# Kernel optimization log

Measured on AMD Instinct MI355X. Metric: run time of the kernel, lower is better.

Reference implementation:

```python
import jax, jax.numpy as jnp
import numpy as np

N, R, H, OUT = 512, 16, 16, 1
EPSILON = 1e-6
CUTOFF = 5.0  # ExpNormalSmearing cutoff_upper (cutoff_lower = 0)


def exp_normal_smearing(dist):
    # dist: (N, N, 1) -> (N, N, R); TorchMD-Net style ExpNormalSmearing
    start = jnp.exp(-CUTOFF)
    means = jnp.linspace(start, 1.0, R, dtype=dist.dtype)
    beta = (2.0 / R * (1.0 - start)) ** -2
    cutoff = 0.5 * (jnp.cos(dist * jnp.pi / CUTOFF) + 1.0) * (dist < CUTOFF)
    return cutoff * jnp.exp(-beta * (jnp.exp(-dist) - means) ** 2)


def setup_inputs() -> dict:
    key = jax.random.key(0)
    ks = jax.random.split(key, 9)
    s_in = 1.0 / np.sqrt(H * H)
    s_h = 1.0 / np.sqrt(H)
    return {
        "x": jax.random.normal(ks[0], (N, 3), jnp.float32) * 1.5,
        "W": jax.random.normal(ks[1], (2, N, R, H), jnp.float32) * 0.1,
        "W1": jax.random.normal(ks[2], (H, H * H), jnp.float32) * s_in,
        "b1": jax.random.normal(ks[3], (H,), jnp.float32) * 0.01,
        "W2": jax.random.normal(ks[4], (4 * R * H, H), jnp.float32) * s_h,
        "W3": jax.random.normal(ks[5], (H, H * H), jnp.float32) * s_in,
        "b3": jax.random.normal(ks[6], (H,), jnp.float32) * 0.01,
        "W4": jax.random.normal(ks[7], (OUT, H), jnp.float32) * s_h,
        "b4": jax.random.normal(ks[8], (OUT,), jnp.float32) * 0.01,
    }


def reference(x, W, W1, b1, W2, W3, b3, W4, b4):
    K, Q = W[0], W[1]                               # (N, R, H) each
    diff = x[:, None, :] - x[None, :, :]            # (N, N, 3)
    nsq = jnp.sum(diff * diff, axis=-1, keepdims=True) + EPSILON
    norm = jnp.sqrt(nsq)                            # (N, N, 1)
    diff = diff / nsq                               # note: divided by squared norm (faithful)
    sm = exp_normal_smearing(norm)                  # (N, N, R)
    basis = sm[..., None] * diff[..., None, :]      # (N, N, R, 3)

    bk = jnp.einsum('ijrb,jrc->icb', basis, K)      # (N, H, 3)
    bq = jnp.einsum('ijrb,jrc->icb', basis, Q)
    att = jnp.einsum('ihb,igb->ihg', bk, bq).reshape(N, H * H)
    att = jax.nn.silu(att @ W1.T + b1) @ W2.T       # (N, 4*R*H), second Linear bias-free

    left, right = att[:, : 2 * R * H], att[:, 2 * R * H:]
    pair = left[:, None, :] + right[None, :, :]     # (N, N, 2*R*H)
    K2 = pair[..., : R * H].reshape(N, N, R, H)
    Q2 = pair[..., R * H:].reshape(N, N, R, H)

    bk = jnp.einsum('ijrb,ijrc->icb', basis, K2)    # (N, H, 3)
    bq = jnp.einsum('ijrb,ijrc->icb', basis, Q2)
    att = jnp.einsum('ihb,igb->ihg', bk, bq).reshape(N, H * H)
    return jax.nn.silu(att @ W3.T + b3) @ W4.T + b4  # (N, OUT)
```

## Files before the change

### kernel.cpp

```cpp
#include <hip/hip_runtime.h>
#include <hip/hip_bf16.h>
#include <math.h>

#define NN 512
#define RR 16
#define HH 16


__global__ __launch_bounds__(512) void junmai_k1(
    const float* __restrict__ x,
    const float* __restrict__ W,
    const float* __restrict__ W1,
    const float* __restrict__ b1,
    const float* __restrict__ W2,
    float* __restrict__ att2)
{
    const int i   = blockIdx.x;
    const int tid = threadIdx.x;
    const int c   = tid & 15;
    const int g   = tid >> 4;

    __shared__ float s_red[32][16][6];
    __shared__ float s_bkq[16][6];
    __shared__ float s_att[256];
    __shared__ float s_a1[16];

    const float xi0 = x[i*3+0];
    const float xi1 = x[i*3+1];
    const float xi2 = x[i*3+2];

    const float start = 0.006737946999085467f;
    const float step  = (1.0f - start) * (1.0f/15.0f);
    const float sb    = 0.125f * (1.0f - start);
    const float beta  = 1.0f / (sb * sb);

    const float* Kp = W;
    const float* Qp = W + NN*RR*HH;

    float ak0=0.f, ak1=0.f, ak2=0.f, aq0=0.f, aq1=0.f, aq2=0.f;

    for (int j = g; j < NN; j += 32) {
        float d0 = xi0 - x[j*3+0];
        float d1 = xi1 - x[j*3+1];
        float d2 = xi2 - x[j*3+2];
        float nsq = fmaf(d0,d0, fmaf(d1,d1, fmaf(d2,d2, 1e-6f)));
        float inv = 1.0f / nsq;
        float nrm = sqrtf(nsq);
        d0 *= inv; d1 *= inv; d2 *= inv;
        float cutv = 0.0f;
        if (nrm < 5.0f) cutv = 0.5f * (cosf(nrm * 0.6283185307179586f) + 1.0f);
        float en = __expf(-nrm);

        const float* kj = Kp + j*256 + c;
        const float* qj = Qp + j*256 + c;
        float tk = 0.f, tq = 0.f;
        #pragma unroll
        for (int r = 0; r < 16; ++r) {
            float m = fmaf(step, (float)r, start);
            float t = en - m;
            float e = __expf(-beta * t * t);
            tk = fmaf(e, kj[r*16], tk);
            tq = fmaf(e, qj[r*16], tq);
        }
        tk *= cutv; tq *= cutv;
        ak0 = fmaf(tk, d0, ak0); ak1 = fmaf(tk, d1, ak1); ak2 = fmaf(tk, d2, ak2);
        aq0 = fmaf(tq, d0, aq0); aq1 = fmaf(tq, d1, aq1); aq2 = fmaf(tq, d2, aq2);
    }

    s_red[g][c][0]=ak0; s_red[g][c][1]=ak1; s_red[g][c][2]=ak2;
    s_red[g][c][3]=aq0; s_red[g][c][4]=aq1; s_red[g][c][5]=aq2;
    __syncthreads();

    if (tid < 96) {
        int cc = tid / 6, s = tid % 6;
        float acc = 0.f;
        #pragma unroll
        for (int gg = 0; gg < 32; ++gg) acc += s_red[gg][cc][s];
        s_bkq[cc][s] = acc;
    }
    __syncthreads();

    if (tid < 256) {
        int h = tid >> 4, g2 = tid & 15;
        s_att[tid] = s_bkq[h][0]*s_bkq[g2][3]
                   + s_bkq[h][1]*s_bkq[g2][4]
                   + s_bkq[h][2]*s_bkq[g2][5];
    }
    __syncthreads();

    if (tid < 16) {
        float z = b1[tid];
        const float* w1r = W1 + tid*256;
        for (int m = 0; m < 256; ++m) z = fmaf(s_att[m], w1r[m], z);
        s_a1[tid] = z / (1.0f + __expf(-z));
    }
    __syncthreads();

    {
        float a[16];
        #pragma unroll
        for (int cc = 0; cc < 16; ++cc) a[cc] = s_a1[cc];
        #pragma unroll
        for (int oo = 0; oo < 2; ++oo) {
            int o = tid + oo*512;
            const float* w2r = W2 + o*16;
            float acc = 0.f;
            #pragma unroll
            for (int cc = 0; cc < 16; ++cc) acc = fmaf(a[cc], w2r[cc], acc);
            att2[i*1024 + o] = acc;
        }
    }
}

__global__ __launch_bounds__(512) void junmai_k2(
    const float* __restrict__ x,
    const float* __restrict__ att2,
    const float* __restrict__ W3,
    const float* __restrict__ b3,
    const float* __restrict__ W4,
    const float* __restrict__ b4,
    float* __restrict__ out)
{
    const int i   = blockIdx.x;
    const int tid = threadIdx.x;
    const int c   = tid & 15;
    const int g   = tid >> 4;

    __shared__ float s_red[32][16][9];
    __shared__ float s_acc[16][9];
    __shared__ float s_att[256];
    __shared__ float s_a1[16];

    const float xi0 = x[i*3+0];
    const float xi1 = x[i*3+1];
    const float xi2 = x[i*3+2];

    const float start = 0.006737946999085467f;
    const float step  = (1.0f - start) * (1.0f/15.0f);
    const float sb    = 0.125f * (1.0f - start);
    const float beta  = 1.0f / (sb * sb);

    float ak0=0.f, ak1=0.f, ak2=0.f, aq0=0.f, aq1=0.f, aq2=0.f;
    float as0=0.f, as1=0.f, as2=0.f;

    const float mc = fmaf(step, (float)c, start);

    for (int j = g; j < NN; j += 32) {
        float d0 = xi0 - x[j*3+0];
        float d1 = xi1 - x[j*3+1];
        float d2 = xi2 - x[j*3+2];
        float nsq = fmaf(d0,d0, fmaf(d1,d1, fmaf(d2,d2, 1e-6f)));
        float inv = 1.0f / nsq;
        float nrm = sqrtf(nsq);
        d0 *= inv; d1 *= inv; d2 *= inv;
        float cutv = 0.0f;
        if (nrm < 5.0f) cutv = 0.5f * (cosf(nrm * 0.6283185307179586f) + 1.0f);
        float en = __expf(-nrm);

        const float* rj = att2 + j*1024 + 512 + c;
        float tk = 0.f, tq = 0.f;
        #pragma unroll
        for (int r = 0; r < 16; ++r) {
            float m = fmaf(step, (float)r, start);
            float t = en - m;
            float e = __expf(-beta * t * t);
            tk = fmaf(e, rj[r*16],     tk);
            tq = fmaf(e, rj[256+r*16], tq);
        }
        tk *= cutv; tq *= cutv;
        float tc  = en - mc;
        float smc = cutv * __expf(-beta * tc * tc);

        ak0 = fmaf(tk, d0, ak0); ak1 = fmaf(tk, d1, ak1); ak2 = fmaf(tk, d2, ak2);
        aq0 = fmaf(tq, d0, aq0); aq1 = fmaf(tq, d1, aq1); aq2 = fmaf(tq, d2, aq2);
        as0 = fmaf(smc,d0, as0); as1 = fmaf(smc,d1, as1); as2 = fmaf(smc,d2, as2);
    }

    s_red[g][c][0]=ak0; s_red[g][c][1]=ak1; s_red[g][c][2]=ak2;
    s_red[g][c][3]=aq0; s_red[g][c][4]=aq1; s_red[g][c][5]=aq2;
    s_red[g][c][6]=as0; s_red[g][c][7]=as1; s_red[g][c][8]=as2;
    __syncthreads();

    if (tid < 144) {
        int cc = tid / 9, s = tid % 9;
        float acc = 0.f;
        #pragma unroll
        for (int gg = 0; gg < 32; ++gg) acc += s_red[gg][cc][s];
        s_acc[cc][s] = acc;
    }
    __syncthreads();

    if (tid < 96) {
        int q  = (tid >= 48) ? 1 : 0;
        int u  = tid - q*48;
        int cc = u / 3, b = u % 3;
        const float* lrow = att2 + i*1024 + q*256 + cc;
        float add = 0.f;
        #pragma unroll
        for (int r = 0; r < 16; ++r) add = fmaf(lrow[r*16], s_acc[r][6+b], add);
        s_acc[cc][q*3 + b] += add;
    }
    __syncthreads();

    if (tid < 256) {
        int h = tid >> 4, g2 = tid & 15;
        s_att[tid] = s_acc[h][0]*s_acc[g2][3]
                   + s_acc[h][1]*s_acc[g2][4]
                   + s_acc[h][2]*s_acc[g2][5];
    }
    __syncthreads();

    if (tid < 16) {
        float z = b3[tid];
        const float* w3r = W3 + tid*256;
        for (int m = 0; m < 256; ++m) z = fmaf(s_att[m], w3r[m], z);
        s_a1[tid] = z / (1.0f + __expf(-z));
    }
    __syncthreads();

    if (tid == 0) {
        float acc = b4[0];
        #pragma unroll
        for (int cc = 0; cc < 16; ++cc) acc = fmaf(s_a1[cc], W4[cc], acc);
        out[i] = acc;
    }
}

extern "C" void kernel_launch(void* const* d_in, const int* in_sizes, int n_in,
                              void* d_out, int out_size, void* d_ws, size_t ws_size,
                              hipStream_t stream) {
    (void)in_sizes; (void)n_in; (void)out_size; (void)ws_size;
    const float* x  = (const float*)d_in[0];
    const float* W  = (const float*)d_in[1];
    const float* W1 = (const float*)d_in[2];
    const float* b1 = (const float*)d_in[3];
    const float* W2 = (const float*)d_in[4];
    const float* W3 = (const float*)d_in[5];
    const float* b3 = (const float*)d_in[6];
    const float* W4 = (const float*)d_in[7];
    const float* b4 = (const float*)d_in[8];
    float* att2 = (float*)d_ws;
    float* out  = (float*)d_out;

    junmai_k1<<<NN, 512, 0, stream>>>(x, W, W1, b1, W2, att2);
    junmai_k2<<<NN, 512, 0, stream>>>(x, att2, W3, b3, W4, b4, out);
}
```

Baseline: 134.6 us.

## Split each stage into register-tiled pairwise kernel and per-row MLP kernel

Each of the two fused kernels is split in two. The first is a pairwise-reduction kernel in which each block handles 4 rows i over a quarter of j. Each thread computes 4 channels with float4 loads and reuses the loaded K/Q values across the 4 rows. The second is a per-row kernel that sums the partials and runs the small MLP with a parallelised W1/W3 dot product. Transcendentals switch to the hardware rsq, exp2 and __cosf intrinsics. The design raises arithmetic reuse of the weight loads and spreads the serial MLP tail across more threads, at the cost of two extra launches, workspace round-trips and high register pressure from 96 to 144 accumulators.

```diff
diff --git a/kernel.cpp b/kernel.cpp
--- a/kernel.cpp
+++ b/kernel.cpp
@@ -3,226 +3,381 @@
 #include <math.h>
 
 #define NN 512
-#define RR 16
-#define HH 16
-
-
-__global__ __launch_bounds__(512) void junmai_k1(
-    const float* __restrict__ x,
-    const float* __restrict__ W,
-    const float* __restrict__ W1,
-    const float* __restrict__ b1,
-    const float* __restrict__ W2,
-    float* __restrict__ att2)
+
+#define START 0.006737946999085467f
+#define STEP  ((1.0f - START) * (1.0f/15.0f))
+#define SB    (0.125f * (1.0f - START))
+#define BETA  (1.0f/(SB*SB))
+#define LOG2E 1.4426950408889634f
+#define NB    (-(BETA)*LOG2E)
+
+__global__ __launch_bounds__(256,2) void k1a(const float* __restrict__ x,
+                                             const float* __restrict__ W,
+                                             float* __restrict__ part1)
 {
-    const int i   = blockIdx.x;
+    const int it = blockIdx.x >> 2, jc = blockIdx.x & 3;
+    const int i0 = it * 4;
     const int tid = threadIdx.x;
-    const int c   = tid & 15;
-    const int g   = tid >> 4;
-
-    __shared__ float s_red[32][16][6];
-    __shared__ float s_bkq[16][6];
+    const int s = tid >> 2, l = tid & 3;
+    const int lane = tid & 63, wv = tid >> 6;
+
+    __shared__ float s_part[4][4][96];
+
+    float xi[4][3];
+    #pragma unroll
+    for (int ii = 0; ii < 4; ++ii) {
+        xi[ii][0] = x[(i0+ii)*3+0];
+        xi[ii][1] = x[(i0+ii)*3+1];
+        xi[ii][2] = x[(i0+ii)*3+2];
+    }
+
+    float acc[96];
+    #pragma unroll
+    for (int v = 0; v < 96; ++v) acc[v] = 0.f;
+
+    const int jbase = jc * 128;
+    for (int jt = 0; jt < 2; ++jt) {
+        const int j = jbase + jt*64 + s;
+        const float xj0 = x[j*3+0], xj1 = x[j*3+1], xj2 = x[j*3+2];
+
+        float d[4][3], cutv[4], en[4];
+        #pragma unroll
+        for (int ii = 0; ii < 4; ++ii) {
+            float d0 = xi[ii][0]-xj0, d1 = xi[ii][1]-xj1, d2 = xi[ii][2]-xj2;
+            float nsq = fmaf(d0,d0, fmaf(d1,d1, fmaf(d2,d2, 1e-6f)));
+            float rs  = __builtin_amdgcn_rsqf(nsq);
+            float nrm = nsq * rs;
+            float inv = rs * rs;
+            d[ii][0] = d0*inv; d[ii][1] = d1*inv; d[ii][2] = d2*inv;
+            float cv = 0.f;
+            if (nrm < 5.0f) cv = 0.5f*(__cosf(nrm*0.6283185307179586f)+1.0f);
+            cutv[ii] = cv;
+            en[ii]   = exp2f(-LOG2E * nrm);
+        }
+
+        const float4* kj = reinterpret_cast<const float4*>(W + j*256 + l*4);
+        const float4* qj = reinterpret_cast<const float4*>(W + NN*256 + j*256 + l*4);
+
+        float tk[4][4], tq[4][4];
+        #pragma unroll
+        for (int ii = 0; ii < 4; ++ii)
+            #pragma unroll
+            for (int e = 0; e < 4; ++e) { tk[ii][e] = 0.f; tq[ii][e] = 0.f; }
+
+        #pragma unroll
+        for (int r = 0; r < 16; ++r) {
+            float4 k4 = kj[r*4];
+            float4 q4 = qj[r*4];
+            const float m = START + STEP * (float)r;
+            #pragma unroll
+            for (int ii = 0; ii < 4; ++ii) {
+                float t = en[ii] - m;
+                float e = exp2f(NB * t * t);
+                tk[ii][0] = fmaf(e, k4.x, tk[ii][0]);
+                tk[ii][1] = fmaf(e, k4.y, tk[ii][1]);
+                tk[ii][2] = fmaf(e, k4.z, tk[ii][2]);
+                tk[ii][3] = fmaf(e, k4.w, tk[ii][3]);
+                tq[ii][0] = fmaf(e, q4.x, tq[ii][0]);
+                tq[ii][1] = fmaf(e, q4.y, tq[ii][1]);
+                tq[ii][2] = fmaf(e, q4.z, tq[ii][2]);
+                tq[ii][3] = fmaf(e, q4.w, tq[ii][3]);
+            }
+        }
+
+        #pragma unroll
+        for (int ii = 0; ii < 4; ++ii) {
+            const float w0 = cutv[ii]*d[ii][0];
+            const float w1 = cutv[ii]*d[ii][1];
+            const float w2 = cutv[ii]*d[ii][2];
+            #pragma unroll
+            for (int e = 0; e < 4; ++e) {
+                acc[ii*24 +      e] = fmaf(w0, tk[ii][e], acc[ii*24 +      e]);
+                acc[ii*24 +  4 + e] = fmaf(w1, tk[ii][e], acc[ii*24 +  4 + e]);
+                acc[ii*24 +  8 + e] = fmaf(w2, tk[ii][e], acc[ii*24 +  8 + e]);
+                acc[ii*24 + 12 + e] = fmaf(w0, tq[ii][e], acc[ii*24 + 12 + e]);
+                acc[ii*24 + 16 + e] = fmaf(w1, tq[ii][e], acc[ii*24 + 16 + e]);
+                acc[ii*24 + 20 + e] = fmaf(w2, tq[ii][e], acc[ii*24 + 20 + e]);
+            }
+        }
+    }
+
+    #pragma unroll
+    for (int v = 0; v < 96; ++v) {
+        float t = acc[v];
+        t += __shfl_xor(t, 4);
+        t += __shfl_xor(t, 8);
+        t += __shfl_xor(t, 16);
+        t += __shfl_xor(t, 32);
+        if (lane < 4) s_part[wv][l][v] = t;
+    }
+    __syncthreads();
+
+    for (int v = tid; v < 384; v += 256) {
+        int i = v / 96, o = v - i*96;
+        int kq = o / 48, rem = o - kq*48;
+        int b = rem >> 4, c = rem & 15;
+        int ll = c >> 2, e = c & 3;
+        int f = i*24 + kq*12 + b*4 + e;
+        float sum = s_part[0][ll][f] + s_part[1][ll][f]
+                  + s_part[2][ll][f] + s_part[3][ll][f];
+        part1[(i0+i)*384 + jc*96 + o] = sum;
+    }
+}
+
+__global__ __launch_bounds__(256) void k1b(const float* __restrict__ part1,
+                                           const float* __restrict__ W1,
+                                           const float* __restrict__ b1,
+                                           const float* __restrict__ W2,
+                                           float* __restrict__ att2)
+{
+    const int i = blockIdx.x;
+    const int tid = threadIdx.x;
+    __shared__ float s_bkq[96];
     __shared__ float s_att[256];
+    __shared__ float s_z[16][16];
     __shared__ float s_a1[16];
 
-    const float xi0 = x[i*3+0];
-    const float xi1 = x[i*3+1];
-    const float xi2 = x[i*3+2];
-
-    const float start = 0.006737946999085467f;
-    const float step  = (1.0f - start) * (1.0f/15.0f);
-    const float sb    = 0.125f * (1.0f - start);
-    const float beta  = 1.0f / (sb * sb);
-
-    const float* Kp = W;
-    const float* Qp = W + NN*RR*HH;
-
-    float ak0=0.f, ak1=0.f, ak2=0.f, aq0=0.f, aq1=0.f, aq2=0.f;
-
-    for (int j = g; j < NN; j += 32) {
-        float d0 = xi0 - x[j*3+0];
-        float d1 = xi1 - x[j*3+1];
-        float d2 = xi2 - x[j*3+2];
-        float nsq = fmaf(d0,d0, fmaf(d1,d1, fmaf(d2,d2, 1e-6f)));
-        float inv = 1.0f / nsq;
-        float nrm = sqrtf(nsq);
-        d0 *= inv; d1 *= inv; d2 *= inv;
-        float cutv = 0.0f;
-        if (nrm < 5.0f) cutv = 0.5f * (cosf(nrm * 0.6283185307179586f) + 1.0f);
-        float en = __expf(-nrm);
-
-        const float* kj = Kp + j*256 + c;
-        const float* qj = Qp + j*256 + c;
-        float tk = 0.f, tq = 0.f;
-        #pragma unroll
-        for (int r = 0; r < 16; ++r) {
-            float m = fmaf(step, (float)r, start);
-            float t = en - m;
-            float e = __expf(-beta * t * t);
-            tk = fmaf(e, kj[r*16], tk);
-            tq = fmaf(e, qj[r*16], tq);
-        }
-        tk *= cutv; tq *= cutv;
-        ak0 = fmaf(tk, d0, ak0); ak1 = fmaf(tk, d1, ak1); ak2 = fmaf(tk, d2, ak2);
-        aq0 = fmaf(tq, d0, aq0); aq1 = fmaf(tq, d1, aq1); aq2 = fmaf(tq, d2, aq2);
-    }
-
-    s_red[g][c][0]=ak0; s_red[g][c][1]=ak1; s_red[g][c][2]=ak2;
-    s_red[g][c][3]=aq0; s_red[g][c][4]=aq1; s_red[g][c][5]=aq2;
-    __syncthreads();
-
     if (tid < 96) {
-        int cc = tid / 6, s = tid % 6;
-        float acc = 0.f;
-        #pragma unroll
-        for (int gg = 0; gg < 32; ++gg) acc += s_red[gg][cc][s];
-        s_bkq[cc][s] = acc;
-    }
-    __syncthreads();
-
-    if (tid < 256) {
-        int h = tid >> 4, g2 = tid & 15;
-        s_att[tid] = s_bkq[h][0]*s_bkq[g2][3]
-                   + s_bkq[h][1]*s_bkq[g2][4]
-                   + s_bkq[h][2]*s_bkq[g2][5];
+        const float* p = part1 + i*384 + tid;
+        s_bkq[tid] = p[0] + p[96] + p[192] + p[288];
+    }
+    __syncthreads();
+
+    {
+        int h = tid >> 4, g = tid & 15;
+        s_att[tid] = s_bkq[     h]*s_bkq[48+     g]
+                   + s_bkq[16 + h]*s_bkq[48+16 + g]
+                   + s_bkq[32 + h]*s_bkq[48+32 + g];
+    }
+    __syncthreads();
+
+    {
+        int h = tid & 15, seg = tid >> 4;
+        const float* w1 = W1 + h*256 + seg*16;
+        const float* a  = s_att + seg*16;
+        float p = 0.f;
+        #pragma unroll
+        for (int k = 0; k < 16; ++k) p = fmaf(a[k], w1[k], p);
+        s_z[seg][h] = p;
     }
     __syncthreads();
 
     if (tid < 16) {
         float z = b1[tid];
-        const float* w1r = W1 + tid*256;
-        for (int m = 0; m < 256; ++m) z = fmaf(s_att[m], w1r[m], z);
+        #pragma unroll
+        for (int seg = 0; seg < 16; ++seg) z += s_z[seg][tid];
         s_a1[tid] = z / (1.0f + __expf(-z));
     }
     __syncthreads();
 
+    float a1[16];
+    #pragma unroll
+    for (int c = 0; c < 16; ++c) a1[c] = s_a1[c];
+    #pragma unroll
+    for (int p = 0; p < 4; ++p) {
+        int o = tid + p*256;
+        const float4* w2 = reinterpret_cast<const float4*>(W2 + o*16);
+        float4 wa = w2[0], wb = w2[1], wc = w2[2], wd = w2[3];
+        float accv = wa.x*a1[0] + wa.y*a1[1] + wa.z*a1[2] + wa.w*a1[3]
+                   + wb.x*a1[4] + wb.y*a1[5] + wb.z*a1[6] + wb.w*a1[7]
+                   + wc.x*a1[8] + wc.y*a1[9] + wc.z*a1[10]+ wc.w*a1[11]
+                   + wd.x*a1[12]+ wd.y*a1[13]+ wd.z*a1[14]+ wd.w*a1[15];
+        att2[i*1024 + o] = accv;
+    }
+}
+
+__global__ __launch_bounds__(256,2) void k2a(const float* __restrict__ x,
+                                             const float* __restrict__ att2,
+                                             float* __restrict__ part2)
+{
+    const int it = blockIdx.x >> 2, jc = blockIdx.x & 3;
+    const int i0 = it * 4;
+    const int tid = threadIdx.x;
+    const int s = tid >> 2, l = tid & 3;
+    const int lane = tid & 63, wv = tid >> 6;
+
+    __shared__ float s_part[4][4][144];
+
+    float xi[4][3];
+    #pragma unroll
+    for (int ii = 0; ii < 4; ++ii) {
+        xi[ii][0] = x[(i0+ii)*3+0];
+        xi[ii][1] = x[(i0+ii)*3+1];
+        xi[ii][2] = x[(i0+ii)*3+2];
+    }
+
+    float acc[144];
+    #pragma unroll
+    for (int v = 0; v < 144; ++v) acc[v] = 0.f;
+
+    const int jbase = jc * 128;
+    for (int jt = 0; jt < 2; ++jt) {
+        const int j = jbase + jt*64 + s;
+        const float xj0 = x[j*3+0], xj1 = x[j*3+1], xj2 = x[j*3+2];
+
+        float d[4][3], cutv[4], en[4];
+        #pragma unroll
+        for (int ii = 0; ii < 4; ++ii) {
+            float d0 = xi[ii][0]-xj0, d1 = xi[ii][1]-xj1, d2 = xi[ii][2]-xj2;
+            float nsq = fmaf(d0,d0, fmaf(d1,d1, fmaf(d2,d2, 1e-6f)));
+            float rs  = __builtin_amdgcn_rsqf(nsq);
+            float nrm = nsq * rs;
+            float inv = rs * rs;
+            d[ii][0] = d0*inv; d[ii][1] = d1*inv; d[ii][2] = d2*inv;
+            float cv = 0.f;
+            if (nrm < 5.0f) cv = 0.5f*(__cosf(nrm*0.6283185307179586f)+1.0f);
+            cutv[ii] = cv;
+            en[ii]   = exp2f(-LOG2E * nrm);
+        }
+
+        const float4* rj = reinterpret_cast<const float4*>(att2 + j*1024 + 512 + l*4);
+
+        float tk[4][4], tq[4][4];
+        #pragma unroll
+        for (int ii = 0; ii < 4; ++ii)
+            #pragma unroll
+            for (int e = 0; e < 4; ++e) { tk[ii][e] = 0.f; tq[ii][e] = 0.f; }
+
+        #pragma unroll
+        for (int r = 0; r < 16; ++r) {
+            float4 k4 = rj[r*4];
+            float4 q4 = rj[64 + r*4];
+            const float m = START + STEP * (float)r;
+            #pragma unroll
+            for (int ii = 0; ii < 4; ++ii) {
+                float t = en[ii] - m;
+                float e = exp2f(NB * t * t);
+                tk[ii][0] = fmaf(e, k4.x, tk[ii][0]);
+                tk[ii][1] = fmaf(e, k4.y, tk[ii][1]);
+                tk[ii][2] = fmaf(e, k4.z, tk[ii][2]);
+                tk[ii][3] = fmaf(e, k4.w, tk[ii][3]);
+                tq[ii][0] = fmaf(e, q4.x, tq[ii][0]);
+                tq[ii][1] = fmaf(e, q4.y, tq[ii][1]);
+                tq[ii][2] = fmaf(e, q4.z, tq[ii][2]);
+                tq[ii][3] = fmaf(e, q4.w, tq[ii][3]);
+                if ((r & 3) == l) {
+                    float es = e * cutv[ii];
+                    const int fb = ii*36 + 24 + (r>>2)*3;
+                    acc[fb+0] = fmaf(es, d[ii][0], acc[fb+0]);
+                    acc[fb+1] = fmaf(es, d[ii][1], acc[fb+1]);
+                    acc[fb+2] = fmaf(es, d[ii][2], acc[fb+2]);
+                }
+            }
+        }
+
+        #pragma unroll
+        for (int ii = 0; ii < 4; ++ii) {
+            const float w0 = cutv[ii]*d[ii][0];
+            const float w1 = cutv[ii]*d[ii][1];
+            const float w2 = cutv[ii]*d[ii][2];
+            #pragma unroll
+            for (int e = 0; e < 4; ++e) {
+                acc[ii*36 +      e] = fmaf(w0, tk[ii][e], acc[ii*36 +      e]);
+                acc[ii*36 +  4 + e] = fmaf(w1, tk[ii][e], acc[ii*36 +  4 + e]);
+                acc[ii*36 +  8 + e] = fmaf(w2, tk[ii][e], acc[ii*36 +  8 + e]);
+                acc[ii*36 + 12 + e] = fmaf(w0, tq[ii][e], acc[ii*36 + 12 + e]);
+                acc[ii*36 + 16 + e] = fmaf(w1, tq[ii][e], acc[ii*36 + 16 + e]);
+                acc[ii*36 + 20 + e] = fmaf(w2, tq[ii][e], acc[ii*36 + 20 + e]);
+            }
+        }
+    }
+
+    #pragma unroll
+    for (int v = 0; v < 144; ++v) {
+        float t = acc[v];
+        t += __shfl_xor(t, 4);
+        t += __shfl_xor(t, 8);
+        t += __shfl_xor(t, 16);
+        t += __shfl_xor(t, 32);
+        if (lane < 4) s_part[wv][l][v] = t;
+    }
+    __syncthreads();
+
+    for (int v = tid; v < 576; v += 256) {
+        int i = v / 144, o = v - i*144;
+        int ll, f;
+        if (o < 96) {
+            int kq = o / 48, rem = o - kq*48;
+            int b = rem >> 4, c = rem & 15;
+            ll = c >> 2;
+            f = i*36 + kq*12 + b*4 + (c & 3);
+        } else {
+            int oS = o - 96;
+            int r = oS / 3, b = oS - r*3;
+            ll = r & 3;
+            f = i*36 + 24 + (r>>2)*3 + b;
+        }
+        float sum = s_part[0][ll][f] + s_part[1][ll][f]
+                  + s_part[2][ll][f] + s_part[3][ll][f];
+        part2[(i0+i)*576 + jc*144 + o] = sum;
+    }
+}
+
+__global__ __launch_bounds__(256) void k2b(const float* __restrict__ att2,
+                                           const float* __restrict__ part2,
+                                           const float* __restrict__ W3,
+                                           const float* __restrict__ b3,
+                                           const float* __restrict__ W4,
+                                           const float* __restrict__ b4,
+                                           float* __restrict__ out)
+{
+    const int i = blockIdx.x;
+    const int tid = threadIdx.x;
+    __shared__ float s_red[144];
+    __shared__ float s_att[256];
+    __shared__ float s_z[16][16];
+    __shared__ float s_a1[16];
+
+    if (tid < 144) {
+        const float* p = part2 + i*576 + tid;
+        s_red[tid] = p[0] + p[144] + p[288] + p[432];
+    }
+    __syncthreads();
+
+    if (tid < 96) {
+        int kq = tid / 48, rem = tid - kq*48;
+        int b = rem >> 4, c = rem & 15;
+        const float* lrow = att2 + i*1024 + kq*256 + c;
+        float add = 0.f;
+        #pragma unroll
+        for (int r = 0; r < 16; ++r)
+            add = fmaf(lrow[r*16], s_red[96 + r*3 + b], add);
+        s_red[tid] += add;
+    }
+    __syncthreads();
+
     {
-        float a[16];
-        #pragma unroll
-        for (int cc = 0; cc < 16; ++cc) a[cc] = s_a1[cc];
-        #pragma unroll
-        for (int oo = 0; oo < 2; ++oo) {
-            int o = tid + oo*512;
-            const float* w2r = W2 + o*16;
-            float acc = 0.f;
-            #pragma unroll
-            for (int cc = 0; cc < 16; ++cc) acc = fmaf(a[cc], w2r[cc], acc);
-            att2[i*1024 + o] = acc;
-        }
-    }
-}
-
-__global__ __launch_bounds__(512) void junmai_k2(
-    const float* __restrict__ x,
-    const float* __restrict__ att2,
-    const float* __restrict__ W3,
-    const float* __restrict__ b3,
-    const float* __restrict__ W4,
-    const float* __restrict__ b4,
-    float* __restrict__ out)
-{
-    const int i   = blockIdx.x;
-    const int tid = threadIdx.x;
-    const int c   = tid & 15;
-    const int g   = tid >> 4;
-
-    __shared__ float s_red[32][16][9];
-    __shared__ float s_acc[16][9];
-    __shared__ float s_att[256];
-    __shared__ float s_a1[16];
-
-    const float xi0 = x[i*3+0];
-    const float xi1 = x[i*3+1];
-    const float xi2 = x[i*3+2];
-
-    const float start = 0.006737946999085467f;
-    const float step  = (1.0f - start) * (1.0f/15.0f);
-    const float sb    = 0.125f * (1.0f - start);
-    const float beta  = 1.0f / (sb * sb);
-
-    float ak0=0.f, ak1=0.f, ak2=0.f, aq0=0.f, aq1=0.f, aq2=0.f;
-    float as0=0.f, as1=0.f, as2=0.f;
-
-    const float mc = fmaf(step, (float)c, start);
-
-    for (int j = g; j < NN; j += 32) {
-        float d0 = xi0 - x[j*3+0];
-        float d1 = xi1 - x[j*3+1];
-        float d2 = xi2 - x[j*3+2];
-        float nsq = fmaf(d0,d0, fmaf(d1,d1, fmaf(d2,d2, 1e-6f)));
-        float inv = 1.0f / nsq;
-        float nrm = sqrtf(nsq);
-        d0 *= inv; d1 *= inv; d2 *= inv;
-        float cutv = 0.0f;
-        if (nrm < 5.0f) cutv = 0.5f * (cosf(nrm * 0.6283185307179586f) + 1.0f);
-        float en = __expf(-nrm);
-
-        const float* rj = att2 + j*1024 + 512 + c;
-        float tk = 0.f, tq = 0.f;
-        #pragma unroll
-        for (int r = 0; r < 16; ++r) {
-            float m = fmaf(step, (float)r, start);
-            float t = en - m;
-            float e = __expf(-beta * t * t);
-            tk = fmaf(e, rj[r*16],     tk);
-            tq = fmaf(e, rj[256+r*16], tq);
-        }
-        tk *= cutv; tq *= cutv;
-        float tc  = en - mc;
-        float smc = cutv * __expf(-beta * tc * tc);
-
-        ak0 = fmaf(tk, d0, ak0); ak1 = fmaf(tk, d1, ak1); ak2 = fmaf(tk, d2, ak2);
-        aq0 = fmaf(tq, d0, aq0); aq1 = fmaf(tq, d1, aq1); aq2 = fmaf(tq, d2, aq2);
-        as0 = fmaf(smc,d0, as0); as1 = fmaf(smc,d1, as1); as2 = fmaf(smc,d2, as2);
-    }
-
-    s_red[g][c][0]=ak0; s_red[g][c][1]=ak1; s_red[g][c][2]=ak2;
-    s_red[g][c][3]=aq0; s_red[g][c][4]=aq1; s_red[g][c][5]=aq2;
-    s_red[g][c][6]=as0; s_red[g][c][7]=as1; s_red[g][c][8]=as2;
-    __syncthreads();
-
-    if (tid < 144) {
-        int cc = tid / 9, s = tid % 9;
-        float acc = 0.f;
-        #pragma unroll
-        for (int gg = 0; gg < 32; ++gg) acc += s_red[gg][cc][s];
-        s_acc[cc][s] = acc;
-    }
-    __syncthreads();
-
-    if (tid < 96) {
-        int q  = (tid >= 48) ? 1 : 0;
-        int u  = tid - q*48;
-        int cc = u / 3, b = u % 3;
-        const float* lrow = att2 + i*1024 + q*256 + cc;
-        float add = 0.f;
-        #pragma unroll
-        for (int r = 0; r < 16; ++r) add = fmaf(lrow[r*16], s_acc[r][6+b], add);
-        s_acc[cc][q*3 + b] += add;
-    }
-    __syncthreads();
-
-    if (tid < 256) {
-        int h = tid >> 4, g2 = tid & 15;
-        s_att[tid] = s_acc[h][0]*s_acc[g2][3]
-                   + s_acc[h][1]*s_acc[g2][4]
-                   + s_acc[h][2]*s_acc[g2][5];
+        int h = tid >> 4, g = tid & 15;
+        s_att[tid] = s_red[     h]*s_red[48+     g]
+                   + s_red[16 + h]*s_red[48+16 + g]
+                   + s_red[32 + h]*s_red[48+32 + g];
+    }
+    __syncthreads();
+
+    {
+        int h = tid & 15, seg = tid >> 4;
+        const float* w3 = W3 + h*256 + seg*16;
+        const float* a  = s_att + seg*16;
+        float p = 0.f;
+        #pragma unroll
+        for (int k = 0; k < 16; ++k) p = fmaf(a[k], w3[k], p);
+        s_z[seg][h] = p;
     }
     __syncthreads();
 
     if (tid < 16) {
         float z = b3[tid];
-        const float* w3r = W3 + tid*256;
-        for (int m = 0; m < 256; ++m) z = fmaf(s_att[m], w3r[m], z);
+        #pragma unroll
+        for (int seg = 0; seg < 16; ++seg) z += s_z[seg][tid];
         s_a1[tid] = z / (1.0f + __expf(-z));
     }
     __syncthreads();
 
     if (tid == 0) {
-        float acc = b4[0];
-        #pragma unroll
-        for (int cc = 0; cc < 16; ++cc) acc = fmaf(s_a1[cc], W4[cc], acc);
-        out[i] = acc;
+        float accv = b4[0];
+        #pragma unroll
+        for (int c = 0; c < 16; ++c) accv = fmaf(s_a1[c], W4[c], accv);
+        out[i] = accv;
     }
 }
 
@@ -239,9 +394,14 @@
     const float* b3 = (const float*)d_in[6];
     const float* W4 = (const float*)d_in[7];
     const float* b4 = (const float*)d_in[8];
-    float* att2 = (float*)d_ws;
-    float* out  = (float*)d_out;
-
-    junmai_k1<<<NN, 512, 0, stream>>>(x, W, W1, b1, W2, att2);
-    junmai_k2<<<NN, 512, 0, stream>>>(x, att2, W3, b3, W4, b4, out);
+
+    float* att2  = (float*)d_ws;
+    float* part1 = att2 + 512*1024;
+    float* part2 = part1 + 512*384;
+    float* out   = (float*)d_out;
+
+    k1a<<<512, 256, 0, stream>>>(x, W, part1);
+    k1b<<<512, 256, 0, stream>>>(part1, W1, b1, W2, att2);
+    k2a<<<512, 256, 0, stream>>>(x, att2, part2);
+    k2b<<<512, 256, 0, stream>>>(att2, part2, W3, b3, W4, b4, out);
 }
```

After: 150.3 us. 11.6% more time.
